# Kernel optimization log

Hardware: AMD Instinct MI355X
Metric: run time of the kernel (lower is better)

## Reference

```python
import jax, jax.numpy as jnp
import numpy as np

SEQ, B, IN, H = 2048, 4096, 1, 32


def setup_inputs() -> dict:
    key = jax.random.key(0)
    ks = jax.random.split(key, 8)
    s_ih = 1.0 / np.sqrt(H)  # torch nn.RNN init scale
    return {
        "x": jax.random.normal(ks[0], (SEQ, B, IN), dtype=jnp.float32),
        "hidden": jnp.zeros((1, B, H), dtype=jnp.float32),
        "W_ih": jax.random.uniform(ks[1], (H, IN), jnp.float32, -s_ih, s_ih),
        "b_ih": jax.random.uniform(ks[2], (H,), jnp.float32, -s_ih, s_ih),
        "W_hh": jax.random.uniform(ks[3], (H, H), jnp.float32, -s_ih, s_ih),
        "b_hh": jax.random.uniform(ks[4], (H,), jnp.float32, -s_ih, s_ih),
        "W_fc": jax.random.uniform(ks[5], (IN, H), jnp.float32, -s_ih, s_ih),
        "b_fc": jax.random.uniform(ks[6], (IN,), jnp.float32, -s_ih, s_ih),
    }


def reference(x, hidden, W_ih, b_ih, W_hh, b_hh, W_fc, b_fc):
    # Elman RNN: h_t = tanh(x_t W_ih^T + b_ih + h_{t-1} W_hh^T + b_hh)
    # Precompute the input projection for all timesteps in one GEMM.
    x_proj = jnp.einsum('sbi,hi->sbh', x, W_ih) + b_ih + b_hh  # (SEQ, B, H)
    h0 = hidden[0]  # (B, H), single layer

    def step(h, xp_t):
        h_new = jnp.tanh(xp_t + h @ W_hh.T)
        return h_new, h_new

    _, outputs = jax.lax.scan(step, h0, x_proj)  # outputs: (SEQ, B, H)
    # Trailing Linear: (SEQ, B, H) -> (SEQ, B, IN)
    return jnp.einsum('sbh,oh->sbo', outputs, W_fc) + b_fc
```

## Files before the change

### kernel.cpp

```cpp
#include <hip/hip_runtime.h>

#define SEQ   2048
#define BATCH 4096
#define HD    32

__device__ __forceinline__ float exp2_fast(float a) {
#if __has_builtin(__builtin_amdgcn_exp2f)
    return __builtin_amdgcn_exp2f(a);
#else
    return exp2f(a);
#endif
}

__device__ __forceinline__ float rcp_fast(float a) {
#if __has_builtin(__builtin_amdgcn_rcpf)
    return __builtin_amdgcn_rcpf(a);
#else
    return 1.0f / a;
#endif
}

__device__ __forceinline__ float fast_tanh(float v) {
    float ax = fabsf(v);
    float e  = exp2_fast(ax * -2.8853900817779268f);
    float r  = (1.0f - e) * rcp_fast(1.0f + e);
    return copysignf(r, v);
}

template <int CTRL>
__device__ __forceinline__ float dpp_x(float v) {
    return __int_as_float(
        __builtin_amdgcn_update_dpp(0, __float_as_int(v), CTRL, 0xF, 0xF, false));
}

__device__ __forceinline__ float swz_xor16(float v) {
    return __int_as_float(__builtin_amdgcn_ds_swizzle(__float_as_int(v), 0x401F));
}

__global__ __launch_bounds__(256, 2) void rnn_elman_kernel(
    const float* __restrict__ x, const float* __restrict__ hidden,
    const float* __restrict__ W_ih, const float* __restrict__ b_ih,
    const float* __restrict__ W_hh, const float* __restrict__ b_hh,
    const float* __restrict__ W_fc, const float* __restrict__ b_fc,
    float* __restrict__ out)
{
    __shared__ float sh[8 * 36];

    const int tid = threadIdx.x;
    const int i   = tid & 31;
    const int ks  = i & 3;
    const int eb  = tid >> 5;
    const int e   = blockIdx.x * 8 + eb;

    float w0[8], w1[8], w2[8], w3[8];
    {
        const int rbase = i & ~3;
        const float* R0 = W_hh + (rbase | (ks ^ 0)) * HD + ks * 8;
        const float* R1 = W_hh + (rbase | (ks ^ 1)) * HD + ks * 8;
        const float* R2 = W_hh + (rbase | (ks ^ 2)) * HD + ks * 8;
        const float* R3 = W_hh + (rbase | (ks ^ 3)) * HD + ks * 8;
        #pragma unroll
        for (int m = 0; m < 8; ++m) {
            w0[m] = R0[m]; w1[m] = R1[m]; w2[m] = R2[m]; w3[m] = R3[m];
        }
    }
    const float wih  = W_ih[i];
    const float bias = b_ih[i] + b_hh[i];
    const float wfc  = W_fc[i];
    const float bfc  = b_fc[0];

    float* slot = sh + eb * 36;
    const float4* rd = reinterpret_cast<const float4*>(slot + ks * 8);

    slot[i] = hidden[e * HD + i];
    __builtin_amdgcn_wave_barrier();
    float4 hb0 = rd[0], hb1 = rd[1];

    float xq0 = x[(size_t)0 * BATCH + e];
    float xq1 = x[(size_t)1 * BATCH + e];
    float xq2 = x[(size_t)2 * BATCH + e];
    float xq3 = x[(size_t)3 * BATCH + e];

    #pragma unroll 4
    for (int t = 0; t < SEQ; ++t) {
        const float xv = xq0;
        xq0 = xq1; xq1 = xq2; xq2 = xq3;
        {
            int tt = t + 4; tt = tt < SEQ ? tt : SEQ - 1;
            const float* xr = x + (size_t)tt * BATCH;
            xq3 = xr[e];
        }

        float p0 = fmaf(xv, wih, bias);
        float p1 = 0.f, p2 = 0.f, p3 = 0.f;
        {
            const float* hv0 = reinterpret_cast<const float*>(&hb0);
            const float* hv1 = reinterpret_cast<const float*>(&hb1);
            #pragma unroll
            for (int m = 0; m < 4; ++m) {
                const float ha = hv0[m];
                const float hc = hv1[m];
                p0 = fmaf(w0[m], ha, p0);
                p1 = fmaf(w1[m], ha, p1);
                p2 = fmaf(w2[m], ha, p2);
                p3 = fmaf(w3[m], ha, p3);
                p0 = fmaf(w0[m + 4], hc, p0);
                p1 = fmaf(w1[m + 4], hc, p1);
                p2 = fmaf(w2[m + 4], hc, p2);
                p3 = fmaf(w3[m + 4], hc, p3);
            }
        }

        const float q0 = p0 + dpp_x<0xB1>(p1);
        const float q1 = p2 + dpp_x<0xB1>(p3);
        const float z  = q0 + dpp_x<0x4E>(q1);
        const float h  = fast_tanh(z);

        slot[i] = h;
        __builtin_amdgcn_wave_barrier();
        hb0 = rd[0]; hb1 = rd[1];

        float u = h * wfc;
        u += dpp_x<0xB1>(u);
        u += dpp_x<0x4E>(u);
        u += dpp_x<0x141>(u);
        u += dpp_x<0x140>(u);
        u += swz_xor16(u);
        if ((tid & 31) == 0) {
            float* orow = out + (size_t)t * BATCH;
            orow[e] = u + bfc;
        }
    }
}

extern "C" void kernel_launch(void* const* d_in, const int* in_sizes, int n_in,
                              void* d_out, int out_size, void* d_ws, size_t ws_size,
                              hipStream_t stream) {
    const float* x    = (const float*)d_in[0];
    const float* hid  = (const float*)d_in[1];
    const float* W_ih = (const float*)d_in[2];
    const float* b_ih = (const float*)d_in[3];
    const float* W_hh = (const float*)d_in[4];
    const float* b_hh = (const float*)d_in[5];
    const float* W_fc = (const float*)d_in[6];
    const float* b_fc = (const float*)d_in[7];
    float* out = (float*)d_out;

    dim3 grid(BATCH / 8);
    dim3 block(256);
    rnn_elman_kernel<<<grid, block, 0, stream>>>(x, hid, W_ih, b_ih, W_hh, b_hh,
                                                 W_fc, b_fc, out);
}
```

Measured before the change: 609.4 us.

## Replace LDS hidden-state exchange with DPP/swizzle register broadcast in recurrence

The per-step LDS round trip (write h, wave barrier, float4 reads) is replaced by cross-lane DPP permutes and one ds_swizzle. Each lane holds a row and its xor-16 partner row of W_hh, laid out so the permuted h values line up with the weights. The output write is deferred by one step so its swizzle stays off the critical path. The aim is a shorter serial dependency chain per timestep, at the cost of many more DPP-fed FMAs and a more intricate lane mapping.

```diff
diff --git a/kernel.cpp b/kernel.cpp
--- a/kernel.cpp
+++ b/kernel.cpp
@@ -37,99 +37,107 @@
     return __int_as_float(__builtin_amdgcn_ds_swizzle(__float_as_int(v), 0x401F));
 }
 
-__global__ __launch_bounds__(256, 2) void rnn_elman_kernel(
+#define ACC16(P0, P1, HS, C7, C8, C15, W)            \
+    P0 = fmaf((HS),            W[0],  P0);           \
+    P0 = fmaf(dpp_x<0xB1>(HS), W[1],  P0);           \
+    P0 = fmaf(dpp_x<0x4E>(HS), W[2],  P0);           \
+    P0 = fmaf(dpp_x<0x1B>(HS), W[3],  P0);           \
+    P0 = fmaf(dpp_x<0x1B>(C7), W[4],  P0);           \
+    P0 = fmaf(dpp_x<0x4E>(C7), W[5],  P0);           \
+    P0 = fmaf(dpp_x<0xB1>(C7), W[6],  P0);           \
+    P0 = fmaf((C7),            W[7],  P0);           \
+    P1 = fmaf((C8),            W[8],  P1);           \
+    P1 = fmaf(dpp_x<0xB1>(C8), W[9],  P1);           \
+    P1 = fmaf(dpp_x<0x4E>(C8), W[10], P1);           \
+    P1 = fmaf(dpp_x<0x1B>(C8), W[11], P1);           \
+    P1 = fmaf(dpp_x<0x1B>(C15),W[12], P1);           \
+    P1 = fmaf(dpp_x<0x4E>(C15),W[13], P1);           \
+    P1 = fmaf(dpp_x<0xB1>(C15),W[14], P1);           \
+    P1 = fmaf((C15),           W[15], P1);
+
+__global__
+__attribute__((amdgpu_flat_work_group_size(256, 256)))
+__attribute__((amdgpu_waves_per_eu(2, 2)))
+void rnn_elman_kernel(
     const float* __restrict__ x, const float* __restrict__ hidden,
     const float* __restrict__ W_ih, const float* __restrict__ b_ih,
     const float* __restrict__ W_hh, const float* __restrict__ b_hh,
     const float* __restrict__ W_fc, const float* __restrict__ b_fc,
     float* __restrict__ out)
 {
-    __shared__ float sh[8 * 36];
-
     const int tid = threadIdx.x;
     const int i   = tid & 31;
-    const int ks  = i & 3;
+    const int L   = i & 15;
+    const int Hh  = i >> 4;
     const int eb  = tid >> 5;
     const int e   = blockIdx.x * 8 + eb;
+    const int rowA  = i;
+    const int rowB  = i ^ 16;
+    const int kbase = 16 * Hh;
 
-    float w0[8], w1[8], w2[8], w3[8];
-    {
-        const int rbase = i & ~3;
-        const float* R0 = W_hh + (rbase | (ks ^ 0)) * HD + ks * 8;
-        const float* R1 = W_hh + (rbase | (ks ^ 1)) * HD + ks * 8;
-        const float* R2 = W_hh + (rbase | (ks ^ 2)) * HD + ks * 8;
-        const float* R3 = W_hh + (rbase | (ks ^ 3)) * HD + ks * 8;
-        #pragma unroll
-        for (int m = 0; m < 8; ++m) {
-            w0[m] = R0[m]; w1[m] = R1[m]; w2[m] = R2[m]; w3[m] = R3[m];
-        }
+    float wa[16], wb[16];
+    #pragma unroll
+    for (int eo = 0; eo < 16; ++eo) {
+        const int kc = kbase + (L ^ eo);
+        wa[eo] = W_hh[rowA * HD + kc];
+        wb[eo] = W_hh[rowB * HD + kc];
     }
-    const float wih  = W_ih[i];
-    const float bias = b_ih[i] + b_hh[i];
-    const float wfc  = W_fc[i];
+    const float wih  = W_ih[rowA];
+    const float bias = b_ih[rowA] + b_hh[rowA];
+    const float wfc  = W_fc[rowA];
     const float bfc  = b_fc[0];
 
-    float* slot = sh + eb * 36;
-    const float4* rd = reinterpret_cast<const float4*>(slot + ks * 8);
-
-    slot[i] = hidden[e * HD + i];
-    __builtin_amdgcn_wave_barrier();
-    float4 hb0 = rd[0], hb1 = rd[1];
+    float h = hidden[e * HD + rowA];
 
     float xq0 = x[(size_t)0 * BATCH + e];
     float xq1 = x[(size_t)1 * BATCH + e];
     float xq2 = x[(size_t)2 * BATCH + e];
     float xq3 = x[(size_t)3 * BATCH + e];
 
+    float u_keep = 0.f, u_swz = 0.f;
+
     #pragma unroll 4
     for (int t = 0; t < SEQ; ++t) {
+        if (t > 0) {
+            const float tot = u_keep + u_swz + bfc;
+            if (i == 0) out[(size_t)(t - 1) * BATCH + e] = tot;
+        }
+
         const float xv = xq0;
         xq0 = xq1; xq1 = xq2; xq2 = xq3;
         {
             int tt = t + 4; tt = tt < SEQ ? tt : SEQ - 1;
-            const float* xr = x + (size_t)tt * BATCH;
-            xq3 = xr[e];
+            xq3 = x[(size_t)tt * BATCH + e];
         }
 
-        float p0 = fmaf(xv, wih, bias);
-        float p1 = 0.f, p2 = 0.f, p3 = 0.f;
-        {
-            const float* hv0 = reinterpret_cast<const float*>(&hb0);
-            const float* hv1 = reinterpret_cast<const float*>(&hb1);
-            #pragma unroll
-            for (int m = 0; m < 4; ++m) {
-                const float ha = hv0[m];
-                const float hc = hv1[m];
-                p0 = fmaf(w0[m], ha, p0);
-                p1 = fmaf(w1[m], ha, p1);
-                p2 = fmaf(w2[m], ha, p2);
-                p3 = fmaf(w3[m], ha, p3);
-                p0 = fmaf(w0[m + 4], hc, p0);
-                p1 = fmaf(w1[m + 4], hc, p1);
-                p2 = fmaf(w2[m + 4], hc, p2);
-                p3 = fmaf(w3[m + 4], hc, p3);
-            }
-        }
+        const float c7  = dpp_x<0x141>(h);
+        const float c15 = dpp_x<0x140>(h);
+        const float c8  = dpp_x<0x141>(c15);
 
-        const float q0 = p0 + dpp_x<0xB1>(p1);
-        const float q1 = p2 + dpp_x<0xB1>(p3);
-        const float z  = q0 + dpp_x<0x4E>(q1);
-        const float h  = fast_tanh(z);
+        float b0 = 0.f, b1 = 0.f;
+        ACC16(b0, b1, h, c7, c8, c15, wb);
+        const float pb   = b0 + b1;
+        const float recv = swz_xor16(pb);
 
-        slot[i] = h;
-        __builtin_amdgcn_wave_barrier();
-        hb0 = rd[0]; hb1 = rd[1];
+        float a0 = fmaf(xv, wih, bias);
+        float a1 = 0.f;
+        ACC16(a0, a1, h, c7, c8, c15, wa);
+
+        const float z = (a0 + a1) + recv;
+        h = fast_tanh(z);
 
         float u = h * wfc;
         u += dpp_x<0xB1>(u);
         u += dpp_x<0x4E>(u);
         u += dpp_x<0x141>(u);
         u += dpp_x<0x140>(u);
-        u += swz_xor16(u);
-        if ((tid & 31) == 0) {
-            float* orow = out + (size_t)t * BATCH;
-            orow[e] = u + bfc;
-        }
+        u_keep = u;
+        u_swz  = swz_xor16(u);
+    }
+
+    {
+        const float tot = u_keep + u_swz + bfc;
+        if (i == 0) out[(size_t)(SEQ - 1) * BATCH + e] = tot;
     }
 }
 
```

Measured after the change: 723.7 us. +18.7%, slower.

## Pack recurrent FMAs into float2 vectors, double block size, reorder LDS exchange

Applied to the files above, without the earlier changes.

Holds the W_hh slices and the hidden state as float2 vectors so the compiler can emit packed FMA instructions (v_pk_fma_f32), roughly halving the VALU instruction count of the 32-wide dot product. The block grows from 8 to 16 sequences (512 threads) with amdgpu_waves_per_eu(2,2), so fewer blocks are launched and occupancy is set explicitly. The output reduction now issues its DPP and swizzle before the LDS write-back of h, so the swizzle latency can overlap the exchange. Packed accumulation adds a final pair-sum per accumulator and changes the floating-point summation order slightly.

```diff
diff --git a/kernel.cpp b/kernel.cpp
--- a/kernel.cpp
+++ b/kernel.cpp
@@ -3,6 +3,9 @@
 #define SEQ   2048
 #define BATCH 4096
 #define HD    32
+
+typedef float f32x2 __attribute__((ext_vector_type(2)));
+typedef float f32x4 __attribute__((ext_vector_type(4)));
 
 __device__ __forceinline__ float exp2_fast(float a) {
 #if __has_builtin(__builtin_amdgcn_exp2f)
@@ -37,31 +40,32 @@
     return __int_as_float(__builtin_amdgcn_ds_swizzle(__float_as_int(v), 0x401F));
 }
 
-__global__ __launch_bounds__(256, 2) void rnn_elman_kernel(
+__global__
+__attribute__((amdgpu_flat_work_group_size(512, 512)))
+__attribute__((amdgpu_waves_per_eu(2, 2)))
+void rnn_elman_kernel(
     const float* __restrict__ x, const float* __restrict__ hidden,
     const float* __restrict__ W_ih, const float* __restrict__ b_ih,
     const float* __restrict__ W_hh, const float* __restrict__ b_hh,
     const float* __restrict__ W_fc, const float* __restrict__ b_fc,
     float* __restrict__ out)
 {
-    __shared__ float sh[8 * 36];
+    __shared__ float sh[16 * 36];
 
     const int tid = threadIdx.x;
     const int i   = tid & 31;
     const int ks  = i & 3;
     const int eb  = tid >> 5;
-    const int e   = blockIdx.x * 8 + eb;
+    const int e   = blockIdx.x * 16 + eb;
 
-    float w0[8], w1[8], w2[8], w3[8];
+    f32x2 wv[4][4];
     {
         const int rbase = i & ~3;
-        const float* R0 = W_hh + (rbase | (ks ^ 0)) * HD + ks * 8;
-        const float* R1 = W_hh + (rbase | (ks ^ 1)) * HD + ks * 8;
-        const float* R2 = W_hh + (rbase | (ks ^ 2)) * HD + ks * 8;
-        const float* R3 = W_hh + (rbase | (ks ^ 3)) * HD + ks * 8;
         #pragma unroll
-        for (int m = 0; m < 8; ++m) {
-            w0[m] = R0[m]; w1[m] = R1[m]; w2[m] = R2[m]; w3[m] = R3[m];
+        for (int j = 0; j < 4; ++j) {
+            const float* R = W_hh + (rbase | (ks ^ j)) * HD + ks * 8;
+            #pragma unroll
+            for (int m = 0; m < 4; ++m) wv[j][m] = f32x2{R[2 * m], R[2 * m + 1]};
         }
     }
     const float wih  = W_ih[i];
@@ -70,16 +74,22 @@
     const float bfc  = b_fc[0];
 
     float* slot = sh + eb * 36;
-    const float4* rd = reinterpret_cast<const float4*>(slot + ks * 8);
+    const f32x4* rd = reinterpret_cast<const f32x4*>(slot + ks * 8);
 
     slot[i] = hidden[e * HD + i];
     __builtin_amdgcn_wave_barrier();
-    float4 hb0 = rd[0], hb1 = rd[1];
+    f32x2 h2[4];
+    {
+        const f32x4 a = rd[0], b = rd[1];
+        h2[0] = f32x2{a.x, a.y}; h2[1] = f32x2{a.z, a.w};
+        h2[2] = f32x2{b.x, b.y}; h2[3] = f32x2{b.z, b.w};
+    }
 
-    float xq0 = x[(size_t)0 * BATCH + e];
-    float xq1 = x[(size_t)1 * BATCH + e];
-    float xq2 = x[(size_t)2 * BATCH + e];
-    float xq3 = x[(size_t)3 * BATCH + e];
+    const float* __restrict__ xe = x + e;
+    float xq0 = xe[(size_t)0 * BATCH];
+    float xq1 = xe[(size_t)1 * BATCH];
+    float xq2 = xe[(size_t)2 * BATCH];
+    float xq3 = xe[(size_t)3 * BATCH];
 
     #pragma unroll 4
     for (int t = 0; t < SEQ; ++t) {
@@ -87,49 +97,45 @@
         xq0 = xq1; xq1 = xq2; xq2 = xq3;
         {
             int tt = t + 4; tt = tt < SEQ ? tt : SEQ - 1;
-            const float* xr = x + (size_t)tt * BATCH;
-            xq3 = xr[e];
+            xq3 = xe[(size_t)tt * BATCH];
         }
 
-        float p0 = fmaf(xv, wih, bias);
-        float p1 = 0.f, p2 = 0.f, p3 = 0.f;
-        {
-            const float* hv0 = reinterpret_cast<const float*>(&hb0);
-            const float* hv1 = reinterpret_cast<const float*>(&hb1);
-            #pragma unroll
-            for (int m = 0; m < 4; ++m) {
-                const float ha = hv0[m];
-                const float hc = hv1[m];
-                p0 = fmaf(w0[m], ha, p0);
-                p1 = fmaf(w1[m], ha, p1);
-                p2 = fmaf(w2[m], ha, p2);
-                p3 = fmaf(w3[m], ha, p3);
-                p0 = fmaf(w0[m + 4], hc, p0);
-                p1 = fmaf(w1[m + 4], hc, p1);
-                p2 = fmaf(w2[m + 4], hc, p2);
-                p3 = fmaf(w3[m + 4], hc, p3);
-            }
+        f32x2 p0 = f32x2{fmaf(xv, wih, bias), 0.f};
+        f32x2 p1 = f32x2{0.f, 0.f};
+        f32x2 p2 = f32x2{0.f, 0.f};
+        f32x2 p3 = f32x2{0.f, 0.f};
+        #pragma unroll
+        for (int m = 0; m < 4; ++m) {
+            const f32x2 hm = h2[m];
+            p0 += wv[0][m] * hm;
+            p1 += wv[1][m] * hm;
+            p2 += wv[2][m] * hm;
+            p3 += wv[3][m] * hm;
         }
+        const float P0 = p0.x + p0.y;
+        const float P1 = p1.x + p1.y;
+        const float P2 = p2.x + p2.y;
+        const float P3 = p3.x + p3.y;
 
-        const float q0 = p0 + dpp_x<0xB1>(p1);
-        const float q1 = p2 + dpp_x<0xB1>(p3);
+        const float q0 = P0 + dpp_x<0xB1>(P1);
+        const float q1 = P2 + dpp_x<0xB1>(P3);
         const float z  = q0 + dpp_x<0x4E>(q1);
         const float h  = fast_tanh(z);
-
-        slot[i] = h;
-        __builtin_amdgcn_wave_barrier();
-        hb0 = rd[0]; hb1 = rd[1];
 
         float u = h * wfc;
         u += dpp_x<0xB1>(u);
         u += dpp_x<0x4E>(u);
         u += dpp_x<0x141>(u);
         u += dpp_x<0x140>(u);
-        u += swz_xor16(u);
-        if ((tid & 31) == 0) {
-            float* orow = out + (size_t)t * BATCH;
-            orow[e] = u + bfc;
-        }
+        const float usw = swz_xor16(u);
+
+        slot[i] = h;
+        __builtin_amdgcn_wave_barrier();
+        const f32x4 a = rd[0], b = rd[1];
+        h2[0] = f32x2{a.x, a.y}; h2[1] = f32x2{a.z, a.w};
+        h2[2] = f32x2{b.x, b.y}; h2[3] = f32x2{b.z, b.w};
+
+        if ((tid & 31) == 0) out[(size_t)t * BATCH + e] = u + usw + bfc;
     }
 }
 
@@ -146,8 +152,8 @@
     const float* b_fc = (const float*)d_in[7];
     float* out = (float*)d_out;
 
-    dim3 grid(BATCH / 8);
-    dim3 block(256);
+    dim3 grid(BATCH / 16);
+    dim3 block(512);
     rnn_elman_kernel<<<grid, block, 0, stream>>>(x, hid, W_ih, b_ih, W_hh, b_hh,
                                                  W_fc, b_fc, out);
 }
```

After: 576.5 us. 5.4% less time.
